# Kernel tuning notes

Hardware: AMD Instinct MI355X
Metric: run time of the kernel (lower is better)

## Reference

```python
import jax, jax.numpy as jnp
import numpy as np

NUM_NODES = 65536       # B * gcn_nodes_num = 256 * 256
NODES_PER_GRAPH = 256
GCN_EMB_DIM = 128
N_EMBD = 512
NUM_EDGES = 1048576     # avg degree 16
NEG_SLOPE = 0.1


def gcn_conv(x, edge_index, W, b, num_nodes):
    """PyG GCNConv: add self-loops, symmetric normalization, linear, aggregate."""
    loop = jnp.arange(num_nodes, dtype=edge_index.dtype)
    src = jnp.concatenate([edge_index[0], loop])
    dst = jnp.concatenate([edge_index[1], loop])
    deg = jax.ops.segment_sum(jnp.ones_like(dst, dtype=x.dtype), dst,
                              num_segments=num_nodes)
    dinv = jnp.where(deg > 0, jax.lax.rsqrt(deg), jnp.zeros_like(deg))
    norm = dinv[src] * dinv[dst]              # [E+N]
    h = x @ W                                 # [N, out]
    msg = h[src] * norm[:, None]              # [E+N, out]
    out = jax.ops.segment_sum(msg, dst, num_segments=num_nodes)
    return out + b


def setup_inputs() -> dict:
    key = jax.random.key(0)
    ks = jax.random.split(key, 8)
    nodes = jax.random.normal(ks[0], (NUM_NODES, 3), dtype=jnp.float32)
    edge_index = jax.random.randint(ks[1], (2, NUM_EDGES), 0, NUM_NODES,
                                    dtype=jnp.int64)
    W1 = jax.random.normal(ks[2], (3, 3), dtype=jnp.float32) * 0.5
    b1 = jnp.zeros((3,), dtype=jnp.float32)
    W2 = jax.random.normal(ks[3], (3, GCN_EMB_DIM), dtype=jnp.float32) * 0.5
    b2 = jnp.zeros((GCN_EMB_DIM,), dtype=jnp.float32)
    W3 = jax.random.normal(ks[4], (GCN_EMB_DIM * NODES_PER_GRAPH, N_EMBD),
                           dtype=jnp.float32) * 0.01
    b3 = jnp.zeros((N_EMBD,), dtype=jnp.float32)
    return {"nodes": nodes, "edge_index": edge_index,
            "W1": W1, "b1": b1, "W2": W2, "b2": b2, "W3": W3, "b3": b3}


def reference(nodes, edge_index, W1, b1, W2, b2, W3, b3):
    n = nodes.shape[0]
    h = gcn_conv(nodes, edge_index, W1, b1, n)           # GCNConv(3,3)
    h = jnp.where(h >= 0, h, NEG_SLOPE * h)              # leaky_relu(0.1)
    h = gcn_conv(h, edge_index, W2, b2, n)               # GCNConv(3,128)
    h = h.reshape(-1, GCN_EMB_DIM * NODES_PER_GRAPH)     # [B, 128*256]
    out = h @ W3 + b3                                    # [B, 512]
    return out
```

## Files before the change

kernel.cpp:

```cpp
#include <hip/hip_runtime.h>

static constexpr int NN   = 65536;
static constexpr int NPG  = 256;
static constexpr int NB   = 256;
static constexpr int EMB  = 128;
static constexpr int NOUT = 512;

static constexpr int NBIN = 256;
static constexpr int CAP  = 4608;
static constexpr int SCAP = CAP + 256;

static constexpr int BT = 8;
static constexpr int KS = 16;
static constexpr int IC = NPG / KS;

__global__ __launch_bounds__(1024)
void k_partV(const int* __restrict__ src, const int* __restrict__ dst, int E,
             int* __restrict__ gbin, int* __restrict__ part,
             const float* __restrict__ W2, const float* __restrict__ b2,
             const float* __restrict__ W3, float4* __restrict__ V4) {
    union SH {
        struct { int hist[NBIN]; int loff[NBIN]; int base[NBIN]; int scanbuf[NBIN];
                 int stage[4096]; } part;
        float4 red[8][4][128];
    };
    __shared__ SH sh;
    int tid = threadIdx.x;
    int bid = blockIdx.x;

    if (bid >= NBIN) {
        int i  = bid - NBIN;
        int j4 = tid & 127;
        int cg = tid >> 7;
        const float4* w3 = (const float4*)(W3 + (size_t)i * EMB * NOUT)
                           + (size_t)cg * 16 * (NOUT/4) + j4;
        float4 a0 = {0,0,0,0}, a1 = {0,0,0,0}, a2 = {0,0,0,0}, a3 = {0,0,0,0};
        for (int c = 0; c < 16; c++) {
            float4 v = w3[(size_t)c * (NOUT/4)];
            int cc = cg*16 + c;
            float w0 = W2[0*EMB+cc], w1 = W2[1*EMB+cc], w2 = W2[2*EMB+cc], wb = b2[cc];
            a0.x += w0*v.x; a0.y += w0*v.y; a0.z += w0*v.z; a0.w += w0*v.w;
            a1.x += w1*v.x; a1.y += w1*v.y; a1.z += w1*v.z; a1.w += w1*v.w;
            a2.x += w2*v.x; a2.y += w2*v.y; a2.z += w2*v.z; a2.w += w2*v.w;
            a3.x += wb*v.x; a3.y += wb*v.y; a3.z += wb*v.z; a3.w += wb*v.w;
        }
        sh.red[cg][0][j4] = a0;
        sh.red[cg][1][j4] = a1;
        sh.red[cg][2][j4] = a2;
        sh.red[cg][3][j4] = a3;
        __syncthreads();
        if (tid < 512) {
            int k = tid >> 7, jj = tid & 127;
            float4 s = sh.red[0][k][jj];
#pragma unroll
            for (int g = 1; g < 8; g++) {
                float4 v = sh.red[g][k][jj];
                s.x += v.x; s.y += v.y; s.z += v.z; s.w += v.w;
            }
            sh.red[0][k][jj] = s;
        }
        __syncthreads();
        if (tid < NOUT) {
            int j = tid;
            const float* r0 = (const float*)&sh.red[0][0][j >> 2];
            const float* r1 = (const float*)&sh.red[0][1][j >> 2];
            const float* r2 = (const float*)&sh.red[0][2][j >> 2];
            const float* r3 = (const float*)&sh.red[0][3][j >> 2];
            float4 o = { r0[j & 3], r1[j & 3], r2[j & 3], r3[j & 3] };
            V4[(size_t)i * NOUT + j] = o;
        }
        return;
    }
    int epb = (E + NBIN - 1) / NBIN;
    int e0 = bid * epb;
    int e1 = min(e0 + epb, E);
    if (tid < NBIN) sh.part.hist[tid] = 0;
    __syncthreads();

    int pk[4], bn[4], rk[4];
    int n = 0;
    int e = e0 + tid * 4;
    if (e + 4 <= e1) {
        int4 s4 = *(const int4*)(src + e);
        int4 d4 = *(const int4*)(dst + e);
        int ss[4] = {s4.x, s4.y, s4.z, s4.w};
        int dd[4] = {d4.x, d4.y, d4.z, d4.w};
#pragma unroll
        for (int k = 0; k < 4; k++) {
            pk[k] = ss[k] | ((dd[k] & 255) << 16);
            bn[k] = dd[k] >> 8;
            rk[k] = atomicAdd(&sh.part.hist[bn[k]], 1);
        }
        n = 4;
    } else {
        for (int k = 0; k < 4 && e + k < e1; k++) {
            int s = src[e+k], d = dst[e+k];
            pk[n] = s | ((d & 255) << 16);
            bn[n] = d >> 8;
            rk[n] = atomicAdd(&sh.part.hist[bn[n]], 1);
            n++;
        }
    }
    __syncthreads();

    if (tid < NBIN) sh.part.scanbuf[tid] = sh.part.hist[tid];
    __syncthreads();
    for (int off = 1; off < NBIN; off <<= 1) {
        int v = 0;
        if (tid < NBIN && tid >= off) v = sh.part.scanbuf[tid - off];
        __syncthreads();
        if (tid < NBIN) sh.part.scanbuf[tid] += v;
        __syncthreads();
    }
    if (tid < NBIN) {
        sh.part.loff[tid] = sh.part.scanbuf[tid] - sh.part.hist[tid];
        sh.part.base[tid] = atomicAdd(&gbin[tid], sh.part.hist[tid]);
    }
    __syncthreads();

    for (int k = 0; k < n; k++) sh.part.stage[sh.part.loff[bn[k]] + rk[k]] = pk[k];
    __syncthreads();

    int bin = tid >> 2;
    int cnt = sh.part.hist[bin], bs = sh.part.base[bin], lo = sh.part.loff[bin];
    for (int t = tid & 3; t < cnt; t += 4) {
        int gp = bs + t;
        if (gp < CAP) part[bin * CAP + gp] = sh.part.stage[lo + t];
    }
}

__global__ __launch_bounds__(512)
void k_csr(const int* __restrict__ gbin, const int* __restrict__ part,
           const float* __restrict__ nodes,
           float* __restrict__ dinv, float4* __restrict__ y1,
           int* __restrict__ rs, unsigned short* __restrict__ srt) {
    __shared__ int pkst[CAP];
    __shared__ int hist[NPG], off_[NPG];
    __shared__ int wtot[4];
    __shared__ unsigned short stageS[SCAP];
    int tid = threadIdx.x, bin = blockIdx.x;
    if (tid < NPG) hist[tid] = 0;
    __syncthreads();
    int cnt = min(gbin[bin], CAP);
    const int* pp = part + (size_t)bin * CAP;
    for (int e = tid; e < cnt; e += 512) {
        int p = pp[e];
        pkst[e] = p;
        atomicAdd(&hist[(p >> 16) & 255], 1);
    }
    __syncthreads();

    int h = 0, v = 0;
    if (tid < NPG) { h = hist[tid]; v = (h + 1) & ~1; }
    int lane = tid & 63;
#pragma unroll
    for (int off = 1; off < 64; off <<= 1) {
        int t = __shfl_up(v, off, 64);
        if (tid < NPG && lane >= off) v += t;
    }
    if (tid < NPG && lane == 63) wtot[tid >> 6] = v;
    __syncthreads();
    if (tid < NPG) {
        int wv = tid >> 6;
        int offs = 0;
#pragma unroll
        for (int w = 0; w < 3; w++) if (w < wv) offs += wtot[w];
        int start = v + offs - ((h + 1) & ~1);
        off_[tid] = start;
        int node = bin * NPG + tid;
        float di = rsqrtf((float)(h + 1));
        dinv[node] = di;
        y1[node] = make_float4(nodes[3*node+0] * di, nodes[3*node+1] * di,
                               nodes[3*node+2] * di, 0.f);
        rs[node] = start | (h << 20);
    }
    __syncthreads();
    for (int e = tid; e < cnt; e += 512) {
        int p = pkst[e];
        int pos = atomicAdd(&off_[(p >> 16) & 255], 1);
        stageS[pos] = (unsigned short)(p & 0xFFFF);
    }
    __syncthreads();
    int tot = wtot[0] + wtot[1] + wtot[2] + wtot[3];
    const unsigned int* so = (const unsigned int*)stageS;
    unsigned int* g = (unsigned int*)(srt + (size_t)bin * SCAP);
    for (int t = tid; t < (tot >> 1); t += 512) g[t] = so[t];
}

__device__ __forceinline__ void agg_pass(int g, const int* __restrict__ rs,
                                         const unsigned short* __restrict__ srt,
                                         const float* __restrict__ dinv,
                                         const float* __restrict__ W1,
                                         const float* __restrict__ b1,
                                         const float4* __restrict__ yin,
                                         float4* __restrict__ yout, bool first) {
    int i = g >> 3, sub = g & 7;
    int rsd = rs[i];
    int start = rsd & 0xFFFFF, deg = rsd >> 20;
    const unsigned int* spw = (const unsigned int*)(srt + (size_t)(i >> 8) * SCAP + start);
    int npairs = (deg + 1) >> 1;
    float ax = 0.f, ay = 0.f, az = 0.f;
    for (int w = sub; w < npairs; w += 8) {
        unsigned int u = spw[w];
        float4 v0 = yin[u & 0xFFFF];
        ax += v0.x; ay += v0.y; az += v0.z;
        if (2*w + 1 < deg) {
            float4 v1 = yin[u >> 16];
            ax += v1.x; ay += v1.y; az += v1.z;
        }
    }
    ax += __shfl_xor(ax, 1); ay += __shfl_xor(ay, 1); az += __shfl_xor(az, 1);
    ax += __shfl_xor(ax, 2); ay += __shfl_xor(ay, 2); az += __shfl_xor(az, 2);
    ax += __shfl_xor(ax, 4); ay += __shfl_xor(ay, 4); az += __shfl_xor(az, 4);
    if (sub == 0) {
        float4 self = yin[i];
        float di = dinv[i];
        float a0 = (ax + self.x) * di, a1 = (ay + self.y) * di, a2 = (az + self.z) * di;
        if (first) {
            float h[3];
#pragma unroll
            for (int k = 0; k < 3; k++) {
                float t = a0 * W1[0*3+k] + a1 * W1[1*3+k] + a2 * W1[2*3+k] + b1[k];
                t = (t >= 0.f) ? t : 0.1f * t;
                h[k] = t * di;
            }
            yout[i] = make_float4(h[0], h[1], h[2], 0.f);
        } else {
            yout[i] = make_float4(a0, a1, a2, 0.f);
        }
    }
}

__global__ void k_agg1(const int* __restrict__ rs, const unsigned short* __restrict__ srt,
                       const float* __restrict__ dinv, const float4* __restrict__ y1,
                       const float* __restrict__ W1, const float* __restrict__ b1,
                       float4* __restrict__ y2) {
    agg_pass(blockIdx.x * 256 + threadIdx.x, rs, srt, dinv, W1, b1, y1, y2, true);
}

__global__ void k_agg2(const int* __restrict__ rs, const unsigned short* __restrict__ srt,
                       const float* __restrict__ dinv, const float4* __restrict__ y2,
                       float4* __restrict__ agg2) {
    agg_pass(blockIdx.x * 256 + threadIdx.x, rs, srt, dinv, nullptr, nullptr,
             y2, agg2, false);
}

__global__ void k_out_part(const float4* __restrict__ agg2, const float4* __restrict__ V4,
                           float* __restrict__ part) {
    __shared__ float4 a_s[BT * IC];
    int tid = threadIdx.x;
    int j  = blockIdx.x * 256 + tid;
    int b0 = blockIdx.y * BT;
    int i0 = blockIdx.z * IC;
    for (int idx = tid; idx < BT * IC; idx += 256) {
        int t = idx / IC, i = idx % IC;
        a_s[idx] = agg2[(size_t)(b0 + t) * NPG + i0 + i];
    }
    __syncthreads();

    float acc[BT];
#pragma unroll
    for (int t = 0; t < BT; t++) acc[t] = 0.f;

    const float4* vj = V4 + (size_t)i0 * NOUT + j;
    for (int i = 0; i < IC; i++) {
        float4 v = vj[(size_t)i * NOUT];
#pragma unroll
        for (int t = 0; t < BT; t++) {
            float4 a = a_s[t*IC + i];
            acc[t] += a.x * v.x + a.y * v.y + a.z * v.z + v.w;
        }
    }
#pragma unroll
    for (int t = 0; t < BT; t++)
        part[((size_t)blockIdx.z * NB + b0 + t) * NOUT + j] = acc[t];
}

__global__ void k_reduce(const float4* __restrict__ part4, const float4* __restrict__ b3_4,
                         float4* __restrict__ out4) {
    int idx = blockIdx.x * 256 + threadIdx.x;
    int j4 = idx & (NOUT/4 - 1);
    float4 acc = b3_4[j4];
#pragma unroll
    for (int s = 0; s < KS; s++) {
        float4 v = part4[(size_t)s * (NB*NOUT/4) + idx];
        acc.x += v.x; acc.y += v.y; acc.z += v.z; acc.w += v.w;
    }
    out4[idx] = acc;
}

extern "C" void kernel_launch(void* const* d_in, const int* in_sizes, int n_in,
                              void* d_out, int out_size, void* d_ws, size_t ws_size,
                              hipStream_t stream) {
    const float* nodes = (const float*)d_in[0];
    const int*   ei    = (const int*)  d_in[1];
    const float* W1    = (const float*)d_in[2];
    const float* b1    = (const float*)d_in[3];
    const float* W2    = (const float*)d_in[4];
    const float* b2    = (const float*)d_in[5];
    const float* W3    = (const float*)d_in[6];
    const float* b3    = (const float*)d_in[7];

    const int E = in_sizes[1] / 2;
    const int* src = ei;
    const int* dst = ei + E;

    char* ws = (char*)d_ws;
    int*    gbin  = (int*)ws;
    float4* y1    = (float4*)(ws + 1024);
    float4* y2    = y1 + NN;
    float4* agg2  = y2 + NN;
    float4* V4    = agg2 + NN;
    float*  partO = (float*)(V4 + (size_t)NPG * NOUT);
    int*    partE = (int*)(partO + (size_t)KS * NB * NOUT);
    unsigned short* srt = (unsigned short*)(partE + (size_t)NBIN * CAP);
    int*    rs    = (int*)(srt + (size_t)NBIN * SCAP);
    float*  dinv  = (float*)(rs + NN);

    hipMemsetAsync(gbin, 0, NBIN * 4, stream);
    k_partV   <<<2*NBIN, 1024, 0, stream>>>(src, dst, E, gbin, partE, W2, b2, W3, V4);
    k_csr     <<<NBIN,    512, 0, stream>>>(gbin, partE, nodes, dinv, y1, rs, srt);
    k_agg1    <<<NN*8/256, 256, 0, stream>>>(rs, srt, dinv, y1, W1, b1, y2);
    k_agg2    <<<NN*8/256, 256, 0, stream>>>(rs, srt, dinv, y2, agg2);
    k_out_part<<<dim3(2, NB/BT, KS), 256, 0, stream>>>(agg2, V4, partO);
    k_reduce  <<<NB*NOUT/4/256,      256, 0, stream>>>((const float4*)partO,
                                                       (const float4*)b3, (float4*)d_out);
}
```

Baseline: 156.5 us.

## Drop global bin atomics and memset; fuse split-K reduce into output kernel

The edge partition kernel no longer reserves space in global bins with atomics. Each block writes its locally sorted chunk contiguously, plus a per-block table of bin offsets and counts. The CSR kernel gathers each bin's pieces from all 256 source blocks using a prefix scan over that table, which removes the memset launch. The separate split-K reduction kernel is replaced by a last-block-done counter inside k_out_part, which also drops one launch; the counter is zeroed by the CSR kernel. The cost is more scattered small reads in the CSR gather and a threadfence/atomic tail on each output tile.

After: 253.4 us. +61.9%, slower.

```diff
diff --git a/kernel.cpp b/kernel.cpp
--- a/kernel.cpp
+++ b/kernel.cpp
@@ -16,11 +16,11 @@
 
 __global__ __launch_bounds__(1024)
 void k_partV(const int* __restrict__ src, const int* __restrict__ dst, int E,
-             int* __restrict__ gbin, int* __restrict__ part,
+             int* __restrict__ part, int* __restrict__ cl,
              const float* __restrict__ W2, const float* __restrict__ b2,
              const float* __restrict__ W3, float4* __restrict__ V4) {
     union SH {
-        struct { int hist[NBIN]; int loff[NBIN]; int base[NBIN]; int scanbuf[NBIN];
+        struct { int hist[NBIN]; int loff[NBIN]; int scanbuf[NBIN];
                  int stage[4096]; } part;
         float4 red[8][4][128];
     };
@@ -113,59 +113,92 @@
         __syncthreads();
     }
     if (tid < NBIN) {
-        sh.part.loff[tid] = sh.part.scanbuf[tid] - sh.part.hist[tid];
-        sh.part.base[tid] = atomicAdd(&gbin[tid], sh.part.hist[tid]);
+        int lo = sh.part.scanbuf[tid] - sh.part.hist[tid];
+        sh.part.loff[tid] = lo;
+        cl[bid * NBIN + tid] = lo | (sh.part.hist[tid] << 16);
     }
     __syncthreads();
 
     for (int k = 0; k < n; k++) sh.part.stage[sh.part.loff[bn[k]] + rk[k]] = pk[k];
     __syncthreads();
 
-    int bin = tid >> 2;
-    int cnt = sh.part.hist[bin], bs = sh.part.base[bin], lo = sh.part.loff[bin];
-    for (int t = tid & 3; t < cnt; t += 4) {
-        int gp = bs + t;
-        if (gp < CAP) part[bin * CAP + gp] = sh.part.stage[lo + t];
-    }
+    int ctot = e1 - e0;
+    for (int t = tid; t < ctot; t += 1024)
+        part[(size_t)bid * epb + t] = sh.part.stage[t];
 }
 
 __global__ __launch_bounds__(512)
-void k_csr(const int* __restrict__ gbin, const int* __restrict__ part,
+void k_csr(const int* __restrict__ cl, const int* __restrict__ part, int epb,
            const float* __restrict__ nodes,
            float* __restrict__ dinv, float4* __restrict__ y1,
-           int* __restrict__ rs, unsigned short* __restrict__ srt) {
+           int* __restrict__ rs, unsigned short* __restrict__ srt,
+           int* __restrict__ cntO) {
     __shared__ int pkst[CAP];
     __shared__ int hist[NPG], off_[NPG];
     __shared__ int wtot[4];
+    __shared__ int cls[NBIN], blo[NBIN];
     __shared__ unsigned short stageS[SCAP];
     int tid = threadIdx.x, bin = blockIdx.x;
+    if (bin == 0 && tid < 64) cntO[tid] = 0;
     if (tid < NPG) hist[tid] = 0;
-    __syncthreads();
-    int cnt = min(gbin[bin], CAP);
-    const int* pp = part + (size_t)bin * CAP;
-    for (int e = tid; e < cnt; e += 512) {
-        int p = pp[e];
-        pkst[e] = p;
-        atomicAdd(&hist[(p >> 16) & 255], 1);
-    }
-    __syncthreads();
-
-    int h = 0, v = 0;
-    if (tid < NPG) { h = hist[tid]; v = (h + 1) & ~1; }
+
+    int cn = 0, v = 0;
+    if (tid < NBIN) {
+        int c = cl[tid * NBIN + bin];
+        cls[tid] = c;
+        cn = c >> 16;
+        v = cn;
+    }
     int lane = tid & 63;
 #pragma unroll
     for (int off = 1; off < 64; off <<= 1) {
         int t = __shfl_up(v, off, 64);
-        if (tid < NPG && lane >= off) v += t;
-    }
-    if (tid < NPG && lane == 63) wtot[tid >> 6] = v;
+        if (tid < NBIN && lane >= off) v += t;
+    }
+    if (tid < NBIN && lane == 63) wtot[tid >> 6] = v;
+    __syncthreads();
+    if (tid < NBIN) {
+        int wv = tid >> 6, offs = 0;
+#pragma unroll
+        for (int w = 0; w < 3; w++) if (w < wv) offs += wtot[w];
+        blo[tid] = v + offs - cn;
+    }
+    __syncthreads();
+    int ctot = wtot[0] + wtot[1] + wtot[2] + wtot[3];
+    if (ctot > CAP) ctot = CAP;
+
+    {
+        int blk = tid >> 1, half = tid & 1;
+        int c = cls[blk];
+        int lo = c & 0xFFFF, cb = c >> 16;
+        int db = blo[blk];
+        const int* q = part + (size_t)blk * epb + lo;
+        for (int t = half; t < cb; t += 2) {
+            int d2 = db + t;
+            if (d2 < CAP) {
+                int p = q[t];
+                pkst[d2] = p;
+                atomicAdd(&hist[(p >> 16) & 255], 1);
+            }
+        }
+    }
+    __syncthreads();
+
+    int h = 0, v2 = 0;
+    if (tid < NPG) { h = hist[tid]; v2 = (h + 1) & ~1; }
+#pragma unroll
+    for (int off = 1; off < 64; off <<= 1) {
+        int t = __shfl_up(v2, off, 64);
+        if (tid < NPG && lane >= off) v2 += t;
+    }
+    if (tid < NPG && lane == 63) wtot[tid >> 6] = v2;
     __syncthreads();
     if (tid < NPG) {
         int wv = tid >> 6;
         int offs = 0;
 #pragma unroll
         for (int w = 0; w < 3; w++) if (w < wv) offs += wtot[w];
-        int start = v + offs - ((h + 1) & ~1);
+        int start = v2 + offs - ((h + 1) & ~1);
         off_[tid] = start;
         int node = bin * NPG + tid;
         float di = rsqrtf((float)(h + 1));
@@ -175,8 +208,8 @@
         rs[node] = start | (h << 20);
     }
     __syncthreads();
-    for (int e = tid; e < cnt; e += 512) {
-        int p = pkst[e];
+    for (int e2 = tid; e2 < ctot; e2 += 512) {
+        int p = pkst[e2];
         int pos = atomicAdd(&off_[(p >> 16) & 255], 1);
         stageS[pos] = (unsigned short)(p & 0xFFFF);
     }
@@ -246,8 +279,10 @@
 }
 
 __global__ void k_out_part(const float4* __restrict__ agg2, const float4* __restrict__ V4,
-                           float* __restrict__ part) {
+                           float* __restrict__ partO, int* __restrict__ cntO,
+                           const float* __restrict__ b3, float* __restrict__ out) {
     __shared__ float4 a_s[BT * IC];
+    __shared__ int lastFlag;
     int tid = threadIdx.x;
     int j  = blockIdx.x * 256 + tid;
     int b0 = blockIdx.y * BT;
@@ -264,29 +299,32 @@
 
     const float4* vj = V4 + (size_t)i0 * NOUT + j;
     for (int i = 0; i < IC; i++) {
-        float4 v = vj[(size_t)i * NOUT];
+        float4 vv = vj[(size_t)i * NOUT];
 #pragma unroll
         for (int t = 0; t < BT; t++) {
             float4 a = a_s[t*IC + i];
-            acc[t] += a.x * v.x + a.y * v.y + a.z * v.z + v.w;
+            acc[t] += a.x * vv.x + a.y * vv.y + a.z * vv.z + vv.w;
         }
     }
 #pragma unroll
     for (int t = 0; t < BT; t++)
-        part[((size_t)blockIdx.z * NB + b0 + t) * NOUT + j] = acc[t];
-}
-
-__global__ void k_reduce(const float4* __restrict__ part4, const float4* __restrict__ b3_4,
-                         float4* __restrict__ out4) {
-    int idx = blockIdx.x * 256 + threadIdx.x;
-    int j4 = idx & (NOUT/4 - 1);
-    float4 acc = b3_4[j4];
-#pragma unroll
-    for (int s = 0; s < KS; s++) {
-        float4 v = part4[(size_t)s * (NB*NOUT/4) + idx];
-        acc.x += v.x; acc.y += v.y; acc.z += v.z; acc.w += v.w;
-    }
-    out4[idx] = acc;
+        partO[((size_t)blockIdx.z * NB + b0 + t) * NOUT + j] = acc[t];
+
+    __threadfence();
+    if (tid == 0) {
+        int prev = atomicAdd(&cntO[blockIdx.y * gridDim.x + blockIdx.x], 1);
+        lastFlag = (prev == KS - 1) ? 1 : 0;
+    }
+    __syncthreads();
+    if (!lastFlag) return;
+    __threadfence();
+#pragma unroll
+    for (int t = 0; t < BT; t++) {
+        float a = b3[j];
+        for (int s = 0; s < KS; s++)
+            a += partO[((size_t)s * NB + b0 + t) * NOUT + j];
+        out[(size_t)(b0 + t) * NOUT + j] = a;
+    }
 }
 
 extern "C" void kernel_launch(void* const* d_in, const int* in_sizes, int n_in,
@@ -304,10 +342,10 @@
     const int E = in_sizes[1] / 2;
     const int* src = ei;
     const int* dst = ei + E;
+    const int epb = (E + NBIN - 1) / NBIN;
 
     char* ws = (char*)d_ws;
-    int*    gbin  = (int*)ws;
-    float4* y1    = (float4*)(ws + 1024);
+    float4* y1    = (float4*)ws;
     float4* y2    = y1 + NN;
     float4* agg2  = y2 + NN;
     float4* V4    = agg2 + NN;
@@ -316,13 +354,13 @@
     unsigned short* srt = (unsigned short*)(partE + (size_t)NBIN * CAP);
     int*    rs    = (int*)(srt + (size_t)NBIN * SCAP);
     float*  dinv  = (float*)(rs + NN);
-
-    hipMemsetAsync(gbin, 0, NBIN * 4, stream);
-    k_partV   <<<2*NBIN, 1024, 0, stream>>>(src, dst, E, gbin, partE, W2, b2, W3, V4);
-    k_csr     <<<NBIN,    512, 0, stream>>>(gbin, partE, nodes, dinv, y1, rs, srt);
+    int*    cl    = (int*)(dinv + NN);
+    int*    cntO  = cl + NBIN * NBIN;
+
+    k_partV   <<<2*NBIN, 1024, 0, stream>>>(src, dst, E, partE, cl, W2, b2, W3, V4);
+    k_csr     <<<NBIN,    512, 0, stream>>>(cl, partE, epb, nodes, dinv, y1, rs, srt, cntO);
     k_agg1    <<<NN*8/256, 256, 0, stream>>>(rs, srt, dinv, y1, W1, b1, y2);
     k_agg2    <<<NN*8/256, 256, 0, stream>>>(rs, srt, dinv, y2, agg2);
-    k_out_part<<<dim3(2, NB/BT, KS), 256, 0, stream>>>(agg2, V4, partO);
-    k_reduce  <<<NB*NOUT/4/256,      256, 0, stream>>>((const float4*)partO,
-                                                       (const float4*)b3, (float4*)d_out);
-}
+    k_out_part<<<dim3(2, NB/BT, KS), 256, 0, stream>>>(agg2, V4, partO, cntO,
+                                                       b3, (float*)d_out);
+}
```
